# Performance work log

Hardware: AMD Instinct MI355X
Metric: run time of the kernel (lower is better)

Reference implementation:

```python
import jax, jax.numpy as jnp
from jax import lax
import numpy as np

B, C, H, W = 4, 128, 256, 256
HEADS = 8
MID = 256


def conv2d(x, w, stride=1, pad=0, groups=1, mode='zeros'):
    if pad:
        m = 'reflect' if mode == 'reflect' else 'constant'
        x = jnp.pad(x, ((0, 0), (0, 0), (pad, pad), (pad, pad)), mode=m)
    return lax.conv_general_dilated(
        x, w, (stride, stride), 'VALID',
        dimension_numbers=('NCHW', 'OIHW', 'NCHW'),
        feature_group_count=groups)


def layernorm(x, w, b, eps=1e-5):
    # torch LayerNorm over channel dim (applied to b (hw) c layout)
    mu = jnp.mean(x, axis=1, keepdims=True)
    var = jnp.mean((x - mu) ** 2, axis=1, keepdims=True)
    xn = (x - mu) * lax.rsqrt(var + eps)
    return xn * w[None, :, None, None] + b[None, :, None, None]


def l2norm(x, eps=1e-12):
    n = jnp.sqrt(jnp.sum(x * x, axis=-1, keepdims=True))
    return x / jnp.maximum(n, eps)


def setup_inputs() -> dict:
    key = jax.random.key(0)
    ks = jax.random.split(key, 20)
    s = 0.02
    inp = {
        'x': jax.random.normal(ks[0], (B, C, H, W), jnp.float32),
        'illu_feat': jax.random.uniform(ks[1], (B, C, H, W), jnp.float32),
        'ln1_w': jnp.ones((C,), jnp.float32),
        'ln1_b': jnp.zeros((C,), jnp.float32),
        'q_w': jax.random.normal(ks[2], (C, 1, 3, 3), jnp.float32) * s,
        'k_w': jax.random.normal(ks[3], (C, C, 3, 3), jnp.float32) * s,
        'v_w': jax.random.normal(ks[4], (C, C, 1, 1), jnp.float32) * s,
        'a1_w': jax.random.normal(ks[5], (C, 1, 3, 3), jnp.float32) * s,
        'a2_w': jax.random.normal(ks[6], (C // 2, C, 1, 1), jnp.float32) * s,
        'a2_b': jnp.zeros((C // 2,), jnp.float32),
        'temp_a': jnp.ones((HEADS, 1, 1), jnp.float32),
        'temp_v': jnp.ones((HEADS, 1, 1), jnp.float32),
        'po_w': jax.random.normal(ks[7], (C, C, 1, 1), jnp.float32) * s,
        'ln2_w': jnp.ones((C,), jnp.float32),
        'ln2_b': jnp.zeros((C,), jnp.float32),
        'p1_w': jax.random.normal(ks[8], (MID, C, 1, 1), jnp.float32) * s,
        'p1_b': jnp.zeros((MID,), jnp.float32),
        'dw_w': jax.random.normal(ks[9], (MID, 1, 3, 3), jnp.float32) * s,
        'dw_b': jnp.zeros((MID,), jnp.float32),
        'p2_w': jax.random.normal(ks[10], (C, MID, 1, 1), jnp.float32) * s,
        'p2_b': jnp.zeros((C,), jnp.float32),
    }
    return inp


def reference(x, illu_feat, ln1_w, ln1_b, q_w, k_w, v_w, a1_w, a2_w, a2_b,
              temp_a, temp_v, po_w, ln2_w, ln2_b, p1_w, p1_b, dw_w, dw_b,
              p2_w, p2_b):
    b, c, h, w = x.shape
    # ---- Attention branch ----
    xn = layernorm(x, ln1_w, ln1_b)
    q = conv2d(xn, q_w, stride=2, pad=1, groups=c, mode='reflect')  # (b,c,h/2,w/2)
    k = conv2d(xn, k_w, stride=2, pad=1, mode='reflect')            # (b,c,h/2,w/2)
    v = conv2d(xn, v_w) * illu_feat                                 # (b,c,h,w)
    a = conv2d(conv2d(xn, a1_w, stride=2, pad=1, groups=c, mode='reflect'), a2_w)
    a = a + a2_b[None, :, None, None]                               # (b,c/2,h/2,w/2)

    h2, w2 = q.shape[-2:]
    l4 = h2 * w2
    cp = c // HEADS            # channels per head (q,k,v)
    ca = (c // 2) // HEADS     # channels per head (a)
    qr = l2norm(q.reshape(b, HEADS, cp, l4))
    kr = l2norm(k.reshape(b, HEADS, cp, l4))
    ar = l2norm(a.reshape(b, HEADS, ca, l4))
    vr = v.reshape(b, HEADS, cp, h * w)

    attn_a = jax.nn.softmax(jnp.einsum('bhcl,bhdl->bhcd', qr, ar) * temp_a, axis=-1)
    attn_k = jax.nn.softmax(jnp.einsum('bhdl,bhcl->bhdc', ar, kr) * temp_v, axis=-1)
    out_v = jnp.einsum('bhdc,bhcm->bhdm', attn_k, vr)   # (b,h,ca,HW)
    out = jnp.einsum('bhcd,bhdm->bhcm', attn_a, out_v)  # (b,h,cp,HW)
    out = out.reshape(b, c, h, w)
    x = x + conv2d(out, po_w)

    # ---- FFN branch ----
    y = layernorm(x, ln2_w, ln2_b)
    y = conv2d(y, p1_w) + p1_b[None, :, None, None]
    y = conv2d(y, dw_w, pad=1, groups=MID) + dw_b[None, :, None, None]
    y = jax.nn.relu(y)
    y = conv2d(y, p2_w) + p2_b[None, :, None, None]
    return x + y
```

## Files before the change

kernel.cpp:

```cpp
#include <hip/hip_runtime.h>

#define BB 4
#define CC 128
#define HH 256
#define WW 256
#define HWSZ 65536
#define H2 128
#define W2 128
#define L4SZ 16384
#define MIDC 256
#define NHEADS 8

typedef __attribute__((ext_vector_type(8))) short short8;
typedef __attribute__((ext_vector_type(4))) short s16x4;
typedef __attribute__((ext_vector_type(4))) float f32x4;
typedef __attribute__((ext_vector_type(4))) unsigned u32x4;
typedef __attribute__((ext_vector_type(2))) unsigned u32x2;

__device__ __forceinline__ short f2bf(float v) {
  unsigned u = __builtin_bit_cast(unsigned, v);
  u += 0x7fffu + ((u >> 16) & 1u);
  return (short)(u >> 16);
}
__device__ __forceinline__ unsigned pk2(float a, float b) {
  return (unsigned)(unsigned short)f2bf(a) | ((unsigned)(unsigned short)f2bf(b) << 16);
}
__device__ __forceinline__ float bflo(unsigned u) { return __builtin_bit_cast(float, u << 16); }
__device__ __forceinline__ float bfhi(unsigned u) { return __builtin_bit_cast(float, u & 0xffff0000u); }
__device__ __forceinline__ float b2f(short s) {
  return __builtin_bit_cast(float, ((unsigned)(unsigned short)s) << 16);
}

__global__ __launch_bounds__(256) void k_ln1(const float* __restrict__ x,
                                             const float* __restrict__ w,
                                             const float* __restrict__ b,
                                             short* __restrict__ xnt) {
  __shared__ float reds[4][64], red2[4][64];
  __shared__ u32x4 tile[1024];
  int blk = blockIdx.x;
  int bi = blk >> 10, p0 = (blk & 1023) * 64;
  int tid = threadIdx.x, pxl = tid & 63, cs = tid >> 6;
  const float* xp = x + (size_t)(bi * CC + cs * 32) * HWSZ + p0 + pxl;
  float v[32];
  float s = 0.f, s2 = 0.f;
#pragma unroll
  for (int j = 0; j < 32; j++) { float t = xp[j * HWSZ]; v[j] = t; s += t; s2 += t * t; }
  reds[cs][pxl] = s; red2[cs][pxl] = s2;
  __syncthreads();
  float st  = reds[0][pxl] + reds[1][pxl] + reds[2][pxl] + reds[3][pxl];
  float s2t = red2[0][pxl] + red2[1][pxl] + red2[2][pxl] + red2[3][pxl];
  float mu = st * (1.f / CC);
  float rstd = rsqrtf(s2t * (1.f / CC) - mu * mu + 1e-5f);
#pragma unroll
  for (int q = 0; q < 4; q++) {
    u32x4 pk;
#pragma unroll
    for (int e = 0; e < 4; e++) {
      int j = q * 8 + e * 2;
      int c = cs * 32 + j;
      pk[e] = pk2((v[j] - mu) * rstd * w[c] + b[c],
                  (v[j + 1] - mu) * rstd * w[c + 1] + b[c + 1]);
    }
    tile[pxl * 16 + ((cs * 4 + q) ^ (pxl & 7))] = pk;
  }
  __syncthreads();
  u32x4* dst = (u32x4*)xnt + (size_t)(bi * HWSZ + p0) * 16;
  for (int it = 0; it < 4; it++) {
    int f = it * 256 + tid;
    int px = f >> 4, gg = f & 15;
    dst[f] = tile[px * 16 + (gg ^ (px & 7))];
  }
}

__global__ __launch_bounds__(256) void k_wcast(const float* __restrict__ kw,
                                               short* __restrict__ wt) {
  int idx = blockIdx.x * 256 + threadIdx.x;
  if (idx >= 9 * 128 * 128) return;
  int ci = idx & 127, co = (idx >> 7) & 127, tap = idx >> 14;
  wt[idx] = f2bf(kw[(co * CC + ci) * 9 + tap]);
}

__global__ __launch_bounds__(256) void k_prep1(const float* __restrict__ vw,
                                               const float* __restrict__ p1w,
                                               const float* __restrict__ lnw,
                                               const float* __restrict__ lnb,
                                               const float* __restrict__ p1b,
                                               const float* __restrict__ p2w,
                                               const float* __restrict__ qw,
                                               const float* __restrict__ a1w,
                                               const float* __restrict__ dww,
                                               short* __restrict__ vwb,
                                               short* __restrict__ w1p,
                                               short* __restrict__ p2wb,
                                               float* __restrict__ s1,
                                               float* __restrict__ s2f,
                                               float* __restrict__ qwt,
                                               float* __restrict__ a1wt,
                                               float* __restrict__ dwwt) {
  int idx = blockIdx.x * 256 + threadIdx.x;
  if (idx < 16384) vwb[idx] = f2bf(vw[idx]);
  int i2 = idx - 16384;
  if (i2 >= 0 && i2 < 32768) { int c = i2 & 127; w1p[i2] = f2bf(p1w[i2] * lnw[c]); }
  int i3 = idx - 49152;
  if (i3 >= 0 && i3 < 32768) p2wb[i3] = f2bf(p2w[i3]);
  int i4 = idx - 81920;
  if (i4 >= 0 && i4 < 256) {
    float a = 0.f, bb2 = 0.f;
    for (int c = 0; c < 128; c++) {
      a   += p1w[i4 * 128 + c] * lnw[c];
      bb2 += p1w[i4 * 128 + c] * lnb[c];
    }
    s1[i4] = a; s2f[i4] = bb2 + p1b[i4];
  }
  int i5 = idx - 82176;
  if (i5 >= 0 && i5 < 1152) { int tap = i5 >> 7, c = i5 & 127; qwt[i5] = qw[c * 9 + tap]; }
  int i6 = idx - 83328;
  if (i6 >= 0 && i6 < 1152) { int tap = i6 >> 7, c = i6 & 127; a1wt[i6] = a1w[c * 9 + tap]; }
  int i7 = idx - 84480;
  if (i7 >= 0 && i7 < 2304) { int tap = i7 / 256, c = i7 - tap * 256; dwwt[i7] = dww[c * 9 + tap]; }
}

__global__ __launch_bounds__(256) void k_prep2(const float* __restrict__ po,
                                               const float* __restrict__ attnA,
                                               const float* __restrict__ attnK,
                                               short* __restrict__ Mb) {
  __shared__ float T[8][16][16];
  int b = blockIdx.x;
  int tid = threadIdx.x;
  for (int i = tid; i < 2048; i += 256) {
    int h = i >> 8, c = (i >> 4) & 15, cc = i & 15;
    float s = 0.f;
#pragma unroll
    for (int d = 0; d < 8; d++)
      s += attnA[((b * 8 + h) * 16 + c) * 8 + d] * attnK[((b * 8 + h) * 8 + d) * 16 + cc];
    T[h][c][cc] = s;
  }
  __syncthreads();
  for (int i = tid; i < 16384; i += 256) {
    int co = i >> 7, cj = i & 127, h = cj >> 4, cc = cj & 15;
    float s = 0.f;
#pragma unroll
    for (int c = 0; c < 16; c++) s += po[co * 128 + h * 16 + c] * T[h][c][cc];
    Mb[b * 16384 + i] = f2bf(s);
  }
}

__global__ __launch_bounds__(256) void k_dwsn(const short* __restrict__ xnt,
                                              const float* __restrict__ qwt,
                                              const float* __restrict__ a1wt,
                                              short* __restrict__ qg,
                                              short* __restrict__ a1g) {
  int blk = blockIdx.x;
  int xg = blk & 1, y = (blk >> 1) & 127, b = blk >> 8;
  int oct = threadIdx.x & 15, pxq = threadIdx.x >> 4;
  int x0 = xg * 64 + pxq * 4;
  float aq[4][8], aa[4][8];
#pragma unroll
  for (int j = 0; j < 4; j++)
#pragma unroll
    for (int c = 0; c < 8; c++) { aq[j][c] = 0.f; aa[j][c] = 0.f; }
#pragma unroll
  for (int tap = 0; tap < 9; tap++) {
    int dy = tap / 3, dx = tap - 3 * dy;
    int ry = 2 * y + dy - 1; ry = ry < 0 ? -ry : ry;
    float4 wq0 = *(const float4*)(qwt + tap * 128 + oct * 8);
    float4 wq1 = *(const float4*)(qwt + tap * 128 + oct * 8 + 4);
    float4 wa0 = *(const float4*)(a1wt + tap * 128 + oct * 8);
    float4 wa1 = *(const float4*)(a1wt + tap * 128 + oct * 8 + 4);
#pragma unroll
    for (int jq = 0; jq < 4; jq++) {
      int ix = 2 * (x0 + jq) + dx - 1; ix = ix < 0 ? -ix : ix;
      short8 xv = *(const short8*)(xnt + (size_t)((b * HWSZ + ry * WW + ix) * CC) + oct * 8);
      float f0 = b2f(xv[0]), f1 = b2f(xv[1]), f2 = b2f(xv[2]), f3 = b2f(xv[3]);
      float f4 = b2f(xv[4]), f5 = b2f(xv[5]), f6 = b2f(xv[6]), f7 = b2f(xv[7]);
      aq[jq][0] += wq0.x * f0; aq[jq][1] += wq0.y * f1; aq[jq][2] += wq0.z * f2; aq[jq][3] += wq0.w * f3;
      aq[jq][4] += wq1.x * f4; aq[jq][5] += wq1.y * f5; aq[jq][6] += wq1.z * f6; aq[jq][7] += wq1.w * f7;
      aa[jq][0] += wa0.x * f0; aa[jq][1] += wa0.y * f1; aa[jq][2] += wa0.z * f2; aa[jq][3] += wa0.w * f3;
      aa[jq][4] += wa1.x * f4; aa[jq][5] += wa1.y * f5; aa[jq][6] += wa1.z * f6; aa[jq][7] += wa1.w * f7;
    }
  }
  int pb = y * 128 + x0;
#pragma unroll
  for (int j = 0; j < 8; j++) {
    s16x4 vq = { f2bf(aq[0][j]), f2bf(aq[1][j]), f2bf(aq[2][j]), f2bf(aq[3][j]) };
    s16x4 va = { f2bf(aa[0][j]), f2bf(aa[1][j]), f2bf(aa[2][j]), f2bf(aa[3][j]) };
    *(s16x4*)(qg  + (size_t)(b * CC + oct * 8 + j) * L4SZ + pb) = vq;
    *(s16x4*)(a1g + (size_t)(b * CC + oct * 8 + j) * L4SZ + pb) = va;
  }
}

__global__ __launch_bounds__(256) void k_kconv_mfma(const short* __restrict__ xnt,
                                                    const short* __restrict__ wt,
                                                    short* __restrict__ kg) {
  __shared__ short8 ldsb[1156];
  int blk = blockIdx.x;
  int bx = blk & 15, by = (blk >> 4) & 15, bi = blk >> 8;
  int r0 = by * 16 - 1, c0 = bx * 16 - 1;
  int lane = threadIdx.x & 63, wv = threadIdx.x >> 6;
  int px0 = wv * 16;
  int pxl = px0 + (lane & 15);
  int py = pxl >> 3, pxx = pxl & 7;
  int g = lane >> 4;
  f32x4 acc[8];
#pragma unroll
  for (int m = 0; m < 8; m++) acc[m] = (f32x4){0.f, 0.f, 0.f, 0.f};
  for (int ci0 = 0; ci0 < CC; ci0 += 32) {
    __syncthreads();
    for (int i = threadIdx.x; i < 1156; i += 256) {
      int p = i >> 2, gg = i & 3;
      int rr = p / 17, cc = p - rr * 17;
      int gr = r0 + rr; gr = gr < 0 ? -gr : gr;
      int gc = c0 + cc; gc = gc < 0 ? -gc : gc;
      int slot = gg ^ ((p >> 1) & 3);
      ldsb[p * 4 + slot] =
          *(const short8*)(xnt + (size_t)((bi * HWSZ + gr * WW + gc) * CC + ci0 + gg * 8));
    }
    __syncthreads();
#pragma unroll
    for (int tap = 0; tap < 9; tap++) {
      int dy = tap / 3, dx = tap - dy * 3;
      int p = (2 * py + dy) * 17 + 2 * pxx + dx;
      int slot = g ^ ((p >> 1) & 3);
      short8 bfrag = ldsb[p * 4 + slot];
      const short* wbase = wt + (tap * 128 + (lane & 15)) * 128 + ci0 + g * 8;
#pragma unroll
      for (int m = 0; m < 8; m++) {
        short8 afrag = *(const short8*)(wbase + m * 16 * 128);
        acc[m] = __builtin_amdgcn_mfma_f32_16x16x32_bf16(afrag, bfrag, acc[m], 0, 0, 0);
      }
    }
  }
  int oy = by * 8 + py, ox = bx * 8 + pxx;
  int rb = g * 4;
#pragma unroll
  for (int m = 0; m < 8; m++)
#pragma unroll
    for (int r = 0; r < 4; r++)
      kg[(size_t)(bi * CC + m * 16 + rb + r) * L4SZ + oy * W2 + ox] = f2bf(acc[m][r]);
}

__global__ __launch_bounds__(256) void k_a2(const short* __restrict__ a1g,
                                            const float* __restrict__ w,
                                            const float* __restrict__ bias,
                                            short* __restrict__ ab) {
  __shared__ float t[CC][64];
  int blk = blockIdx.x;
  int bi = blk >> 8;
  int p0 = (blk & 255) * 64;
  for (int i = threadIdx.x; i < CC * 64; i += 256) {
    int ci = i >> 6, px = i & 63;
    t[ci][px] = b2f(a1g[(size_t)(bi * CC + ci) * L4SZ + p0 + px]);
  }
  __syncthreads();
  int px = threadIdx.x & 63;
  int co0 = ((__builtin_amdgcn_readfirstlane((int)threadIdx.x)) >> 6) << 4;
  float acc[16];
#pragma unroll
  for (int j = 0; j < 16; j++) acc[j] = 0.f;
  for (int ci = 0; ci < CC; ci++) {
    float in = t[ci][px];
#pragma unroll
    for (int j = 0; j < 16; j++) acc[j] += w[(co0 + j) * CC + ci] * in;
  }
#pragma unroll
  for (int j = 0; j < 16; j++)
    ab[(size_t)(bi * 64 + co0 + j) * L4SZ + p0 + px] = f2bf(acc[j] + bias[co0 + j]);
}

__global__ __launch_bounds__(256) void k_gram(const short* __restrict__ qg,
                                              const short* __restrict__ kg,
                                              const short* __restrict__ ag,
                                              float* __restrict__ partial) {
  __shared__ float red[4][1280];
  int blk = blockIdx.x;
  int bh = blk >> 3, chunk = blk & 7;
  int b = bh >> 3, h = bh & 7;
  int tid = threadIdx.x, lane = tid & 63, wv = tid >> 6;
  int cl = lane & 15, g = lane >> 4;
  const short* qb = qg + (size_t)(b * 128 + h * 16 + cl) * L4SZ;
  const short* kb = kg + (size_t)(b * 128 + h * 16 + cl) * L4SZ;
  const short* ar = ag + (size_t)(b * 64 + h * 8 + cl) * L4SZ;
  int k0 = chunk * 2048 + wv * 512 + g * 8;
  f32x4 t0 = {0,0,0,0}, t1 = {0,0,0,0}, t2 = {0,0,0,0}, t3 = {0,0,0,0}, t4 = {0,0,0,0};
#pragma unroll 4
  for (int ks = 0; ks < 16; ks++) {
    int ko = k0 + ks * 32;
    short8 fq = *(const short8*)(qb + ko);
    short8 fk = *(const short8*)(kb + ko);
    short8 fa = *(const short8*)(ar + ko);
    t0 = __builtin_amdgcn_mfma_f32_16x16x32_bf16(fq, fa, t0, 0, 0, 0);
    t1 = __builtin_amdgcn_mfma_f32_16x16x32_bf16(fa, fk, t1, 0, 0, 0);
    t2 = __builtin_amdgcn_mfma_f32_16x16x32_bf16(fq, fq, t2, 0, 0, 0);
    t3 = __builtin_amdgcn_mfma_f32_16x16x32_bf16(fk, fk, t3, 0, 0, 0);
    t4 = __builtin_amdgcn_mfma_f32_16x16x32_bf16(fa, fa, t4, 0, 0, 0);
  }
#pragma unroll
  for (int r = 0; r < 4; r++) {
    int flat = (g * 4 + r) * 16 + cl;
    red[wv][flat]        = t0[r];
    red[wv][256 + flat]  = t1[r];
    red[wv][512 + flat]  = t2[r];
    red[wv][768 + flat]  = t3[r];
    red[wv][1024 + flat] = t4[r];
  }
  __syncthreads();
  float* po = partial + (size_t)(bh * 8 + chunk) * 1280;
  for (int i = tid; i < 1280; i += 256)
    po[i] = red[0][i] + red[1][i] + red[2][i] + red[3][i];
}

__global__ __launch_bounds__(64) void k_softmax2(const float* __restrict__ partial,
                                                 const float* __restrict__ tA,
                                                 const float* __restrict__ tV,
                                                 float* __restrict__ attnA,
                                                 float* __restrict__ attnK) {
  __shared__ float S[1280];
  int bh = blockIdx.x;
  int h = bh & 7;
  for (int i = threadIdx.x; i < 1280; i += 64) {
    float s = 0.f;
    for (int c = 0; c < 8; c++) s += partial[(size_t)(bh * 8 + c) * 1280 + i];
    S[i] = s;
  }
  __syncthreads();
  float ta = tA[h], tv = tV[h];
  if (threadIdx.x < 16) {
    int c = threadIdx.x;
    float nq = fmaxf(sqrtf(S[512 + c * 17]), 1e-12f);
    float lg[8]; float m = -1e30f;
#pragma unroll
    for (int e = 0; e < 8; e++) {
      float na = fmaxf(sqrtf(S[1024 + e * 17]), 1e-12f);
      lg[e] = S[c * 16 + e] / (nq * na) * ta;
      m = fmaxf(m, lg[e]);
    }
    float sum = 0.f;
#pragma unroll
    for (int e = 0; e < 8; e++) { lg[e] = expf(lg[e] - m); sum += lg[e]; }
    float inv = 1.f / sum;
#pragma unroll
    for (int e = 0; e < 8; e++) attnA[(bh * 16 + c) * 8 + e] = lg[e] * inv;
  } else if (threadIdx.x < 24) {
    int e = threadIdx.x - 16;
    float na = fmaxf(sqrtf(S[1024 + e * 17]), 1e-12f);
    float lg[16]; float m = -1e30f;
#pragma unroll
    for (int c = 0; c < 16; c++) {
      float nk = fmaxf(sqrtf(S[768 + c * 17]), 1e-12f);
      lg[c] = S[256 + e * 16 + c] / (na * nk) * tv;
      m = fmaxf(m, lg[c]);
    }
    float sum = 0.f;
#pragma unroll
    for (int c = 0; c < 16; c++) { lg[c] = expf(lg[c] - m); sum += lg[c]; }
    float inv = 1.f / sum;
#pragma unroll
    for (int c = 0; c < 16; c++) attnK[(bh * 8 + e) * 16 + c] = lg[c] * inv;
  }
}

__global__ __launch_bounds__(256) void k_vx2(const short* __restrict__ xnt,
                                             const float* __restrict__ illu,
                                             const float* __restrict__ x,
                                             const short* __restrict__ vwb,
                                             const short* __restrict__ Mb,
                                             u32x4* __restrict__ x2n4,
                                             float* __restrict__ mu,
                                             float* __restrict__ rs) {
  __shared__ unsigned lds[4608];
  int blk = blockIdx.x;
  int bi = blk >> 10, p0 = (blk & 1023) * 64;
  int tid = threadIdx.x, lane = tid & 63, wv = tid >> 6;
  int cl = lane & 15, g = lane >> 4;
  int px = wv * 16 + cl;
  float ilv[32];
#pragma unroll
  for (int m = 0; m < 8; m++)
#pragma unroll
    for (int r = 0; r < 4; r++)
      ilv[m * 4 + r] = illu[(size_t)(bi * CC + m * 16 + g * 4 + r) * HWSZ + p0 + px];
  const u32x4* xsrc = (const u32x4*)(xnt + ((size_t)(bi * HWSZ + p0) << 7));
  for (int it = 0; it < 4; it++) {
    int idx = it * 256 + tid;
    int pp = idx >> 4, gg = idx & 15;
    u32x4 v = xsrc[pp * 16 + gg];
    ((u32x4*)lds)[pp * 16 + (gg ^ (pp & 7))] = v;
  }
  __syncthreads();
  f32x4 acc[8];
#pragma unroll
  for (int m = 0; m < 8; m++) acc[m] = (f32x4){0.f, 0.f, 0.f, 0.f};
#pragma unroll
  for (int kc = 0; kc < 4; kc++) {
    short8 bf = *(const short8*)((const short*)lds + px * 128 + (((kc * 4 + g) ^ (px & 7)) * 8));
#pragma unroll
    for (int m = 0; m < 8; m++) {
      short8 af = *(const short8*)(vwb + (m * 16 + cl) * 128 + kc * 32 + g * 8);
      acc[m] = __builtin_amdgcn_mfma_f32_16x16x32_bf16(af, bf, acc[m], 0, 0, 0);
    }
  }
  __syncthreads();
#pragma unroll
  for (int m = 0; m < 8; m++) {
    float v0 = acc[m][0] * ilv[m * 4 + 0];
    float v1 = acc[m][1] * ilv[m * 4 + 1];
    float v2 = acc[m][2] * ilv[m * 4 + 2];
    float v3 = acc[m][3] * ilv[m * 4 + 3];
    int gi = 2 * m + (g >> 1);
    unsigned* dst = lds + px * 64 + ((gi ^ (px & 7)) << 2) + (g & 1) * 2;
    dst[0] = pk2(v0, v1);
    dst[1] = pk2(v2, v3);
  }
  __syncthreads();
  float xv[32];
#pragma unroll
  for (int m = 0; m < 8; m++)
#pragma unroll
    for (int r = 0; r < 4; r++)
      xv[m * 4 + r] = x[(size_t)(bi * CC + m * 16 + g * 4 + r) * HWSZ + p0 + px];
  f32x4 acc2[8];
#pragma unroll
  for (int m = 0; m < 8; m++) acc2[m] = (f32x4){0.f, 0.f, 0.f, 0.f};
  const short* Mbb = Mb + bi * 16384;
#pragma unroll
  for (int kc = 0; kc < 4; kc++) {
    short8 bf = *(const short8*)((const short*)lds + px * 128 + (((kc * 4 + g) ^ (px & 7)) * 8));
#pragma unroll
    for (int m = 0; m < 8; m++) {
      short8 af = *(const short8*)(Mbb + (m * 16 + cl) * 128 + kc * 32 + g * 8);
      acc2[m] = __builtin_amdgcn_mfma_f32_16x16x32_bf16(af, bf, acc2[m], 0, 0, 0);
    }
  }
  float s = 0.f, s2 = 0.f;
  unsigned xp[16];
#pragma unroll
  for (int m = 0; m < 8; m++) {
    float tv[4];
#pragma unroll
    for (int r = 0; r < 4; r++) {
      float t = xv[m * 4 + r] + acc2[m][r];
      tv[r] = t; s += t; s2 += t * t;
    }
    xp[2 * m]     = pk2(tv[0], tv[1]);
    xp[2 * m + 1] = pk2(tv[2], tv[3]);
  }
  s  += __shfl_xor(s, 16);  s  += __shfl_xor(s, 32);
  s2 += __shfl_xor(s2, 16); s2 += __shfl_xor(s2, 32);
  float muv = s * (1.f / 128.f);
  float rsv = rsqrtf(s2 * (1.f / 128.f) - muv * muv + 1e-5f);
  if (g == 0) { mu[bi * HWSZ + p0 + px] = muv; rs[bi * HWSZ + p0 + px] = rsv; }
  __syncthreads();
#pragma unroll
  for (int m = 0; m < 8; m++) {
    lds[px * 68 + m * 8 + g * 2 + 0] = xp[2 * m];
    lds[px * 68 + m * 8 + g * 2 + 1] = xp[2 * m + 1];
  }
  __syncthreads();
  u32x4* dst4 = x2n4 + (size_t)(bi * HWSZ + p0) * 16;
  for (int it = 0; it < 4; it++) {
    int flat = it * 256 + tid;
    int pp = flat >> 4, j = flat & 15;
    dst4[flat] = *(const u32x4*)(lds + pp * 68 + j * 4);
  }
}

__global__ __launch_bounds__(256) void k_p1(const u32x4* __restrict__ x2n4,
                                            const short* __restrict__ w1p,
                                            const float* __restrict__ s1,
                                            const float* __restrict__ s2f,
                                            const float* __restrict__ mu,
                                            const float* __restrict__ rs,
                                            u32x4* __restrict__ y1n4) {
  __shared__ u32x4 bt[1024];
  __shared__ u32x4 olds[2048];
  int blk = blockIdx.x;
  int bi = blk >> 10, p0 = (blk & 1023) * 64;
  int tid = threadIdx.x, lane = tid & 63, wv = tid >> 6;
  int cl = lane & 15, g = lane >> 4;
  for (int f = tid; f < 1024; f += 256) {
    int px = f >> 4, kg = f & 15;
    bt[kg * 64 + (px ^ kg)] = x2n4[(size_t)(bi * HWSZ + p0 + px) * 16 + kg];
  }
  __syncthreads();
  f32x4 acc[4][4];
#pragma unroll
  for (int mt = 0; mt < 4; mt++)
#pragma unroll
    for (int n = 0; n < 4; n++) acc[mt][n] = (f32x4){0.f, 0.f, 0.f, 0.f};
#pragma unroll
  for (int kc = 0; kc < 4; kc++) {
    short8 bfr[4];
#pragma unroll
    for (int n = 0; n < 4; n++) {
      int px = n * 16 + cl, kgi = kc * 4 + g;
      bfr[n] = __builtin_bit_cast(short8, bt[kgi * 64 + (px ^ kgi)]);
    }
#pragma unroll
    for (int mt = 0; mt < 4; mt++) {
      short8 af = *(const short8*)(w1p + (wv * 64 + mt * 16 + cl) * 128 + kc * 32 + g * 8);
#pragma unroll
      for (int n = 0; n < 4; n++)
        acc[mt][n] = __builtin_amdgcn_mfma_f32_16x16x32_bf16(af, bfr[n], acc[mt][n], 0, 0, 0);
    }
  }
  float muv[4], rsv[4];
#pragma unroll
  for (int n = 0; n < 4; n++) {
    muv[n] = mu[bi * HWSZ + p0 + n * 16 + cl];
    rsv[n] = rs[bi * HWSZ + p0 + n * 16 + cl];
  }
#pragma unroll
  for (int mt = 0; mt < 4; mt++) {
    int mid = wv * 64 + mt * 16 + g * 4;
    float4 s1v = *(const float4*)(s1 + mid);
    float4 s2v = *(const float4*)(s2f + mid);
    int gi = wv * 8 + mt * 2 + (g >> 1);
#pragma unroll
    for (int n = 0; n < 4; n++) {
      int px = n * 16 + cl;
      float y0 = rsv[n] * (acc[mt][n][0] - muv[n] * s1v.x) + s2v.x;
      float y1 = rsv[n] * (acc[mt][n][1] - muv[n] * s1v.y) + s2v.y;
      float y2 = rsv[n] * (acc[mt][n][2] - muv[n] * s1v.z) + s2v.z;
      float y3 = rsv[n] * (acc[mt][n][3] - muv[n] * s1v.w) + s2v.w;
      unsigned* dp = (unsigned*)&olds[px * 32 + (gi ^ (px & 7))] + (g & 1) * 2;
      dp[0] = pk2(y0, y1);
      dp[1] = pk2(y2, y3);
    }
  }
  __syncthreads();
  u32x4* dst = y1n4 + (size_t)(bi * HWSZ + p0) * 32;
  for (int it = 0; it < 8; it++) {
    int f = it * 256 + tid;
    int px = f >> 5, gi = f & 31;
    dst[f] = olds[px * 32 + (gi ^ (px & 7))];
  }
}

__global__ __launch_bounds__(256) void k_ffn2(const u32x4* __restrict__ y1n4,
                                              const float* __restrict__ dwwt,
                                              const float* __restrict__ dwb,
                                              const short* __restrict__ p2wb,
                                              const float* __restrict__ p2b,
                                              const u32x4* __restrict__ x2n4,
                                              float* __restrict__ out) {
  __shared__ u32x4 ylds[800];
  __shared__ u32x4 dwt[512];
  int blk = blockIdx.x;
  int tx = blk & 31, ty = (blk >> 5) & 31, b = blk >> 10;
  int r0 = ty * 8 - 1, c0 = tx * 8 - 1;
  int tid = threadIdx.x, lane = tid & 63, wv = tid >> 6;
  int cl = lane & 15, g = lane >> 4;
  int pp = tid & 63;
  int qy = pp >> 3, qx = pp & 7;
  int ppsw = (pp ^ (pp >> 3)) & 7;
  f32x4 acc[2][4];
#pragma unroll
  for (int mt = 0; mt < 2; mt++)
#pragma unroll
    for (int n = 0; n < 4; n++) acc[mt][n] = (f32x4){0.f, 0.f, 0.f, 0.f};
  for (int ch = 0; ch < 4; ch++) {
    for (int i = tid; i < 800; i += 256) {
      int p = i >> 3, gg = i & 7;
      int rr = p / 10, cc = p - rr * 10;
      int gr = r0 + rr, gc = c0 + cc;
      u32x4 v = (u32x4){0u, 0u, 0u, 0u};
      if (gr >= 0 && gr < HH && gc >= 0 && gc < WW)
        v = y1n4[(size_t)(b * HWSZ + gr * WW + gc) * 32 + ch * 8 + gg];
      ylds[p * 8 + (gg ^ ((p * 3) & 7))] = v;
    }
    __syncthreads();
#pragma unroll
    for (int e = 0; e < 2; e++) {
      int gran = wv * 2 + e;
      float sdw[8];
#pragma unroll
      for (int j = 0; j < 8; j++) sdw[j] = 0.f;
#pragma unroll
      for (int tap = 0; tap < 9; tap++) {
        int dy = tap / 3, dx = tap - 3 * dy;
        int p = (qy + dy) * 10 + qx + dx;
        u32x4 vv = ylds[p * 8 + (gran ^ ((p * 3) & 7))];
        const float* wp = dwwt + tap * 256 + ch * 64 + gran * 8;
        sdw[0] += wp[0] * bflo(vv.x);
        sdw[1] += wp[1] * bfhi(vv.x);
        sdw[2] += wp[2] * bflo(vv.y);
        sdw[3] += wp[3] * bfhi(vv.y);
        sdw[4] += wp[4] * bflo(vv.z);
        sdw[5] += wp[5] * bfhi(vv.z);
        sdw[6] += wp[6] * bflo(vv.w);
        sdw[7] += wp[7] * bfhi(vv.w);
      }
      const float* db = dwb + ch * 64 + gran * 8;
      u32x4 pkv;
      pkv.x = pk2(fmaxf(sdw[0] + db[0], 0.f), fmaxf(sdw[1] + db[1], 0.f));
      pkv.y = pk2(fmaxf(sdw[2] + db[2], 0.f), fmaxf(sdw[3] + db[3], 0.f));
      pkv.z = pk2(fmaxf(sdw[4] + db[4], 0.f), fmaxf(sdw[5] + db[5], 0.f));
      pkv.w = pk2(fmaxf(sdw[6] + db[6], 0.f), fmaxf(sdw[7] + db[7], 0.f));
      dwt[pp * 8 + (gran ^ ppsw)] = pkv;
    }
    __syncthreads();
#pragma unroll
    for (int kc = 0; kc < 2; kc++) {
      short8 af0 = *(const short8*)(p2wb + (wv * 32 + cl) * 256 + ch * 64 + kc * 32 + g * 8);
      short8 af1 = *(const short8*)(p2wb + (wv * 32 + 16 + cl) * 256 + ch * 64 + kc * 32 + g * 8);
      int gi = kc * 4 + g;
#pragma unroll
      for (int n = 0; n < 4; n++) {
        int px = n * 16 + cl;
        short8 bf = __builtin_bit_cast(short8, dwt[px * 8 + (gi ^ ((px ^ (px >> 3)) & 7))]);
        acc[0][n] = __builtin_amdgcn_mfma_f32_16x16x32_bf16(af0, bf, acc[0][n], 0, 0, 0);
        acc[1][n] = __builtin_amdgcn_mfma_f32_16x16x32_bf16(af1, bf, acc[1][n], 0, 0, 0);
      }
    }
    __syncthreads();
  }
#pragma unroll
  for (int mt = 0; mt < 2; mt++) {
    int cob = wv * 32 + mt * 16 + g * 4;
    float pb0 = p2b[cob + 0], pb1 = p2b[cob + 1], pb2 = p2b[cob + 2], pb3 = p2b[cob + 3];
#pragma unroll
    for (int n = 0; n < 4; n++) {
      int px = n * 16 + cl;
      int oy = ty * 8 + (px >> 3), ox = tx * 8 + (px & 7);
      size_t gp = (size_t)b * HWSZ + oy * WW + ox;
      const unsigned* xr = (const unsigned*)(x2n4 + gp * 16 + (cob >> 3));
      unsigned xa = xr[(g & 1) * 2 + 0], xb2 = xr[(g & 1) * 2 + 1];
      size_t gi = (size_t)(b * CC + cob) * HWSZ + oy * WW + ox;
      out[gi]             = bflo(xa)  + acc[mt][n][0] + pb0;
      out[gi + HWSZ]      = bfhi(xa)  + acc[mt][n][1] + pb1;
      out[gi + 2 * HWSZ]  = bflo(xb2) + acc[mt][n][2] + pb2;
      out[gi + 3 * HWSZ]  = bfhi(xb2) + acc[mt][n][3] + pb3;
    }
  }
}

extern "C" void kernel_launch(void* const* d_in, const int* in_sizes, int n_in,
                              void* d_out, int out_size, void* d_ws, size_t ws_size,
                              hipStream_t stream) {
  const float* x    = (const float*)d_in[0];
  const float* illu = (const float*)d_in[1];
  const float* ln1w = (const float*)d_in[2];
  const float* ln1b = (const float*)d_in[3];
  const float* qw   = (const float*)d_in[4];
  const float* kw   = (const float*)d_in[5];
  const float* vw   = (const float*)d_in[6];
  const float* a1w  = (const float*)d_in[7];
  const float* a2w  = (const float*)d_in[8];
  const float* a2b  = (const float*)d_in[9];
  const float* tA   = (const float*)d_in[10];
  const float* tV   = (const float*)d_in[11];
  const float* pow_ = (const float*)d_in[12];
  const float* ln2w = (const float*)d_in[13];
  const float* ln2b = (const float*)d_in[14];
  const float* p1w  = (const float*)d_in[15];
  const float* p1b  = (const float*)d_in[16];
  const float* dww  = (const float*)d_in[17];
  const float* dwb  = (const float*)d_in[18];
  const float* p2w  = (const float*)d_in[19];
  const float* p2b  = (const float*)d_in[20];
  float* out = (float*)d_out;

  float* ws    = (float*)d_ws;
  u32x4* x2n4  = (u32x4*)ws;
  float* mu    = ws + 16777216;
  float* rs    = ws + 17039360;
  float* attnA = ws + 17301504;
  float* attnK = ws + 17305600;
  short* vwb   = (short*)(ws + 17309696);
  short* w1p   = (short*)(ws + 17317888);
  short* p2wb  = (short*)(ws + 17334272);
  short* Mb    = (short*)(ws + 17350656);
  float* s1    = ws + 17383424;
  float* s2f   = ws + 17383680;
  short* wt    = (short*)(ws + 17383936);
  float* qwt   = ws + 17457664;
  float* a1wt  = ws + 17458816;
  float* dwwt  = ws + 17459968;
  u32x4* y1n4  = (u32x4*)(ws + 17462272);
  short* xnt   = (short*)(ws + 17462272);
  short* qg    = (short*)(ws + 34239488);
  short* kgb   = (short*)(ws + 38433792);
  short* a1g   = (short*)(ws + 42628096);
  short* ab    = (short*)(ws + 46822400);
  float* partial = ws + 48919552;

  k_ln1<<<4096, 256, 0, stream>>>(x, ln1w, ln1b, xnt);
  k_wcast<<<576, 256, 0, stream>>>(kw, wt);
  k_prep1<<<340, 256, 0, stream>>>(vw, p1w, ln2w, ln2b, p1b, p2w, qw, a1w, dww,
                                   vwb, w1p, p2wb, s1, s2f, qwt, a1wt, dwwt);
  k_dwsn<<<1024, 256, 0, stream>>>(xnt, qwt, a1wt, qg, a1g);
  k_kconv_mfma<<<1024, 256, 0, stream>>>(xnt, wt, kgb);
  k_a2<<<1024, 256, 0, stream>>>(a1g, a2w, a2b, ab);
  k_gram<<<256, 256, 0, stream>>>(qg, kgb, ab, partial);
  k_softmax2<<<32, 64, 0, stream>>>(partial, tA, tV, attnA, attnK);
  k_prep2<<<4, 256, 0, stream>>>(pow_, attnA, attnK, Mb);
  k_vx2<<<4096, 256, 0, stream>>>(xnt, illu, x, vwb, Mb, x2n4, mu, rs);
  k_p1<<<4096, 256, 0, stream>>>(x2n4, w1p, s1, s2f, mu, rs, y1n4);
  k_ffn2<<<4096, 256, 0, stream>>>(y1n4, dwwt, dwb, p2wb, p2b, x2n4, out);
}
```

Baseline: 761.9 us.

## Store FFN mid activations in channel-group-major layout and halve ffn2 channel passes

The intermediate p1 output changes from pixel-major (32 granules per pixel) to granule-plane-major, so each 8-channel group is a contiguous plane across pixels. k_ffn2 now processes 128 channels per pass (2 passes instead of 4), using doubled LDS buffers and fewer barriers. It also stages the x2n4 residual tile through LDS for coalesced loads instead of scattered global reads. The gains are fewer synchronisations and contiguous halo loads, traded for higher LDS use per block (lower occupancy) and removed XOR swizzles, which may bring back bank conflicts.

```diff
diff --git a/kernel.cpp b/kernel.cpp
--- a/kernel.cpp
+++ b/kernel.cpp
@@ -470,7 +470,7 @@
                                             const float* __restrict__ s2f,
                                             const float* __restrict__ mu,
                                             const float* __restrict__ rs,
-                                            u32x4* __restrict__ y1n4) {
+                                            u32x4* __restrict__ y1g) {
   __shared__ u32x4 bt[1024];
   __shared__ u32x4 olds[2048];
   int blk = blockIdx.x;
@@ -522,29 +522,28 @@
       float y1 = rsv[n] * (acc[mt][n][1] - muv[n] * s1v.y) + s2v.y;
       float y2 = rsv[n] * (acc[mt][n][2] - muv[n] * s1v.z) + s2v.z;
       float y3 = rsv[n] * (acc[mt][n][3] - muv[n] * s1v.w) + s2v.w;
-      unsigned* dp = (unsigned*)&olds[px * 32 + (gi ^ (px & 7))] + (g & 1) * 2;
+      unsigned* dp = (unsigned*)&olds[gi * 64 + px] + (g & 1) * 2;
       dp[0] = pk2(y0, y1);
       dp[1] = pk2(y2, y3);
     }
   }
   __syncthreads();
-  u32x4* dst = y1n4 + (size_t)(bi * HWSZ + p0) * 32;
   for (int it = 0; it < 8; it++) {
     int f = it * 256 + tid;
-    int px = f >> 5, gi = f & 31;
-    dst[f] = olds[px * 32 + (gi ^ (px & 7))];
-  }
-}
-
-__global__ __launch_bounds__(256) void k_ffn2(const u32x4* __restrict__ y1n4,
+    int gi = f >> 6, px = f & 63;
+    y1g[(size_t)gi * (BB * HWSZ) + bi * HWSZ + p0 + px] = olds[gi * 64 + px];
+  }
+}
+
+__global__ __launch_bounds__(256) void k_ffn2(const u32x4* __restrict__ y1g,
                                               const float* __restrict__ dwwt,
                                               const float* __restrict__ dwb,
                                               const short* __restrict__ p2wb,
                                               const float* __restrict__ p2b,
                                               const u32x4* __restrict__ x2n4,
                                               float* __restrict__ out) {
-  __shared__ u32x4 ylds[800];
-  __shared__ u32x4 dwt[512];
+  __shared__ u32x4 ylds[1600];
+  __shared__ u32x4 dwt[1024];
   int blk = blockIdx.x;
   int tx = blk & 31, ty = (blk >> 5) & 31, b = blk >> 10;
   int r0 = ty * 8 - 1, c0 = tx * 8 - 1;
@@ -552,26 +551,26 @@
   int cl = lane & 15, g = lane >> 4;
   int pp = tid & 63;
   int qy = pp >> 3, qx = pp & 7;
-  int ppsw = (pp ^ (pp >> 3)) & 7;
   f32x4 acc[2][4];
 #pragma unroll
   for (int mt = 0; mt < 2; mt++)
 #pragma unroll
     for (int n = 0; n < 4; n++) acc[mt][n] = (f32x4){0.f, 0.f, 0.f, 0.f};
-  for (int ch = 0; ch < 4; ch++) {
-    for (int i = tid; i < 800; i += 256) {
-      int p = i >> 3, gg = i & 7;
+  for (int ch = 0; ch < 2; ch++) {
+    if (ch) __syncthreads();
+    for (int i = tid; i < 1600; i += 256) {
+      int gg = i / 100, p = i - gg * 100;
       int rr = p / 10, cc = p - rr * 10;
       int gr = r0 + rr, gc = c0 + cc;
       u32x4 v = (u32x4){0u, 0u, 0u, 0u};
       if (gr >= 0 && gr < HH && gc >= 0 && gc < WW)
-        v = y1n4[(size_t)(b * HWSZ + gr * WW + gc) * 32 + ch * 8 + gg];
-      ylds[p * 8 + (gg ^ ((p * 3) & 7))] = v;
+        v = y1g[(size_t)(ch * 16 + gg) * (BB * HWSZ) + b * HWSZ + gr * WW + gc];
+      ylds[gg * 100 + p] = v;
     }
     __syncthreads();
 #pragma unroll
-    for (int e = 0; e < 2; e++) {
-      int gran = wv * 2 + e;
+    for (int e = 0; e < 4; e++) {
+      int gran = wv * 4 + e;
       float sdw[8];
 #pragma unroll
       for (int j = 0; j < 8; j++) sdw[j] = 0.f;
@@ -579,8 +578,8 @@
       for (int tap = 0; tap < 9; tap++) {
         int dy = tap / 3, dx = tap - 3 * dy;
         int p = (qy + dy) * 10 + qx + dx;
-        u32x4 vv = ylds[p * 8 + (gran ^ ((p * 3) & 7))];
-        const float* wp = dwwt + tap * 256 + ch * 64 + gran * 8;
+        u32x4 vv = ylds[gran * 100 + p];
+        const float* wp = dwwt + tap * 256 + ch * 128 + gran * 8;
         sdw[0] += wp[0] * bflo(vv.x);
         sdw[1] += wp[1] * bfhi(vv.x);
         sdw[2] += wp[2] * bflo(vv.y);
@@ -590,41 +589,47 @@
         sdw[6] += wp[6] * bflo(vv.w);
         sdw[7] += wp[7] * bfhi(vv.w);
       }
-      const float* db = dwb + ch * 64 + gran * 8;
+      const float* db = dwb + ch * 128 + gran * 8;
       u32x4 pkv;
       pkv.x = pk2(fmaxf(sdw[0] + db[0], 0.f), fmaxf(sdw[1] + db[1], 0.f));
       pkv.y = pk2(fmaxf(sdw[2] + db[2], 0.f), fmaxf(sdw[3] + db[3], 0.f));
       pkv.z = pk2(fmaxf(sdw[4] + db[4], 0.f), fmaxf(sdw[5] + db[5], 0.f));
       pkv.w = pk2(fmaxf(sdw[6] + db[6], 0.f), fmaxf(sdw[7] + db[7], 0.f));
-      dwt[pp * 8 + (gran ^ ppsw)] = pkv;
+      dwt[gran * 64 + pp] = pkv;
     }
     __syncthreads();
 #pragma unroll
-    for (int kc = 0; kc < 2; kc++) {
-      short8 af0 = *(const short8*)(p2wb + (wv * 32 + cl) * 256 + ch * 64 + kc * 32 + g * 8);
-      short8 af1 = *(const short8*)(p2wb + (wv * 32 + 16 + cl) * 256 + ch * 64 + kc * 32 + g * 8);
+    for (int kc = 0; kc < 4; kc++) {
+      short8 af0 = *(const short8*)(p2wb + (wv * 32 + cl) * 256 + ch * 128 + kc * 32 + g * 8);
+      short8 af1 = *(const short8*)(p2wb + (wv * 32 + 16 + cl) * 256 + ch * 128 + kc * 32 + g * 8);
       int gi = kc * 4 + g;
 #pragma unroll
       for (int n = 0; n < 4; n++) {
         int px = n * 16 + cl;
-        short8 bf = __builtin_bit_cast(short8, dwt[px * 8 + (gi ^ ((px ^ (px >> 3)) & 7))]);
+        short8 bf = __builtin_bit_cast(short8, dwt[gi * 64 + px]);
         acc[0][n] = __builtin_amdgcn_mfma_f32_16x16x32_bf16(af0, bf, acc[0][n], 0, 0, 0);
         acc[1][n] = __builtin_amdgcn_mfma_f32_16x16x32_bf16(af1, bf, acc[1][n], 0, 0, 0);
       }
     }
-    __syncthreads();
-  }
+  }
+  __syncthreads();
+  for (int f = tid; f < 1024; f += 256) {
+    int pxa = f >> 4, gg = f & 15;
+    u32x4 v = x2n4[(size_t)(b * HWSZ + (ty * 8 + (pxa >> 3)) * WW + tx * 8 + (pxa & 7)) * 16 + gg];
+    ylds[gg * 64 + (pxa ^ (gg & 7))] = v;
+  }
+  __syncthreads();
 #pragma unroll
   for (int mt = 0; mt < 2; mt++) {
     int cob = wv * 32 + mt * 16 + g * 4;
+    int q = cob >> 3;
     float pb0 = p2b[cob + 0], pb1 = p2b[cob + 1], pb2 = p2b[cob + 2], pb3 = p2b[cob + 3];
 #pragma unroll
     for (int n = 0; n < 4; n++) {
       int px = n * 16 + cl;
+      const unsigned* xr = (const unsigned*)&ylds[q * 64 + (px ^ (q & 7))] + (g & 1) * 2;
+      unsigned xa = xr[0], xb2 = xr[1];
       int oy = ty * 8 + (px >> 3), ox = tx * 8 + (px & 7);
-      size_t gp = (size_t)b * HWSZ + oy * WW + ox;
-      const unsigned* xr = (const unsigned*)(x2n4 + gp * 16 + (cob >> 3));
-      unsigned xa = xr[(g & 1) * 2 + 0], xb2 = xr[(g & 1) * 2 + 1];
       size_t gi = (size_t)(b * CC + cob) * HWSZ + oy * WW + ox;
       out[gi]             = bflo(xa)  + acc[mt][n][0] + pb0;
       out[gi + HWSZ]      = bfhi(xa)  + acc[mt][n][1] + pb1;
@@ -676,7 +681,7 @@
   float* qwt   = ws + 17457664;
   float* a1wt  = ws + 17458816;
   float* dwwt  = ws + 17459968;
-  u32x4* y1n4  = (u32x4*)(ws + 17462272);
+  u32x4* y1g   = (u32x4*)(ws + 17462272);
   short* xnt   = (short*)(ws + 17462272);
   short* qg    = (short*)(ws + 34239488);
   short* kgb   = (short*)(ws + 38433792);
@@ -695,6 +700,6 @@
   k_softmax2<<<32, 64, 0, stream>>>(partial, tA, tV, attnA, attnK);
   k_prep2<<<4, 256, 0, stream>>>(pow_, attnA, attnK, Mb);
   k_vx2<<<4096, 256, 0, stream>>>(xnt, illu, x, vwb, Mb, x2n4, mu, rs);
-  k_p1<<<4096, 256, 0, stream>>>(x2n4, w1p, s1, s2f, mu, rs, y1n4);
-  k_ffn2<<<4096, 256, 0, stream>>>(y1n4, dwwt, dwb, p2wb, p2b, x2n4, out);
-}
+  k_p1<<<4096, 256, 0, stream>>>(x2n4, w1p, s1, s2f, mu, rs, y1g);
+  k_ffn2<<<4096, 256, 0, stream>>>(y1g, dwwt, dwb, p2wb, p2b, x2n4, out);
+}
```

Result: no change. 769.5 us (+1.0%).
